# Kernel optimization log

Measured on AMD Instinct MI355X. Metric: run time of the kernel, lower is better.

## Reference

```python
import math
import jax, jax.numpy as jnp
from jax import lax
import numpy as np

B, DIM, H, W = 8, 256, 64, 64
D_STATE, D_CONV, EXPAND = 16, 4, 2
D_INNER = EXPAND * DIM
DT_RANK = math.ceil(DIM / 16)
POS_LEN = 16
EPS = 1e-5
GN_GROUPS = 32


def setup_inputs() -> dict:
    key = jax.random.key(0)
    ks = iter(jax.random.split(key, 24))
    rn = lambda shape, s=0.02: jax.random.normal(next(ks), shape, jnp.float32) * s
    inp = {}
    inp["x"] = jax.random.normal(next(ks), (B, DIM, H, W), jnp.float32)
    inp["pos_emb"] = rn((1, DIM, POS_LEN), 1.0)
    inp["ln_g"] = jnp.ones((DIM,), jnp.float32)
    inp["ln_b"] = jnp.zeros((DIM,), jnp.float32)
    inp["m_in_w"] = rn((2, 2 * D_INNER, DIM))
    inp["m_conv_w"] = rn((2, D_INNER, D_CONV), 0.1)
    inp["m_conv_b"] = jnp.zeros((2, D_INNER), jnp.float32)
    inp["m_xproj_w"] = rn((2, DT_RANK + 2 * D_STATE, D_INNER))
    inp["m_dt_w"] = rn((2, D_INNER, DT_RANK), 0.1)
    inp["m_dt_b"] = rn((2, D_INNER), 0.1)
    inp["m_A_log"] = jnp.tile(jnp.log(jnp.arange(1, D_STATE + 1, dtype=jnp.float32))[None, None, :], (2, D_INNER, 1))
    inp["m_D"] = jnp.ones((2, D_INNER), jnp.float32)
    inp["m_out_w"] = rn((2, DIM, D_INNER))
    inp["proj_w"] = rn((DIM, 2 * DIM))
    inp["proj_b"] = jnp.zeros((DIM,), jnp.float32)
    inp["up_dw_w"] = rn((DIM, 1, 3, 3), 0.1)
    inp["up_bn1_g"] = jnp.ones((DIM,), jnp.float32)
    inp["up_bn1_b"] = jnp.zeros((DIM,), jnp.float32)
    inp["up_pw_w"] = rn((DIM, DIM), 0.05)
    inp["up_bn2_g"] = jnp.ones((DIM,), jnp.float32)
    inp["up_bn2_b"] = jnp.zeros((DIM,), jnp.float32)
    inp["down_pw_w"] = rn((DIM, DIM), 0.05)
    inp["down_bn_g"] = jnp.ones((DIM,), jnp.float32)
    inp["down_bn_b"] = jnp.zeros((DIM,), jnp.float32)
    inp["gn_g"] = jnp.ones((DIM,), jnp.float32)
    inp["gn_b"] = jnp.zeros((DIM,), jnp.float32)
    return inp


def reference(x, pos_emb, ln_g, ln_b, m_in_w, m_conv_w, m_conv_b, m_xproj_w, m_dt_w, m_dt_b,
              m_A_log, m_D, m_out_w, proj_w, proj_b, up_dw_w, up_bn1_g, up_bn1_b, up_pw_w,
              up_bn2_g, up_bn2_b, down_pw_w, down_bn_g, down_bn_b, gn_g, gn_b):
    Bx, C, Hh, Ww = x.shape

    def ln(t):  # LayerNorm over last dim (shared self.norm)
        m = jnp.mean(t, -1, keepdims=True)
        v = jnp.mean((t - m) ** 2, -1, keepdims=True)
        return (t - m) * lax.rsqrt(v + EPS) * ln_g + ln_b

    def bn(t, g, b):  # BatchNorm2d in eval mode with default running stats (mean 0, var 1)
        return t * (g / jnp.sqrt(1.0 + EPS))[None, :, None, None] + b[None, :, None, None]

    def gn(t):  # GroupNorm(32, C), shared params (self.bn)
        Bn, Cn, Hn, Wn = t.shape
        tg = t.reshape(Bn, GN_GROUPS, Cn // GN_GROUPS, Hn, Wn)
        m = jnp.mean(tg, (2, 3, 4), keepdims=True)
        v = jnp.mean((tg - m) ** 2, (2, 3, 4), keepdims=True)
        tg = (tg - m) * lax.rsqrt(v + EPS)
        return tg.reshape(Bn, Cn, Hn, Wn) * gn_g[None, :, None, None] + gn_b[None, :, None, None]

    def interp_pos(N):  # F.interpolate(pos_embed, size=N, mode='linear', align_corners=False)
        coords = jnp.maximum((jnp.arange(N, dtype=jnp.float32) + 0.5) * (POS_LEN / N) - 0.5, 0.0)
        i0 = jnp.floor(coords).astype(jnp.int32)
        i1 = jnp.minimum(i0 + 1, POS_LEN - 1)
        wgt = coords - i0.astype(jnp.float32)
        return pos_emb[:, :, i0] * (1.0 - wgt) + pos_emb[:, :, i1] * wgt  # (1,C,N)

    def pe_branch(vals, idx, N):  # vals (B,C,N); indices interp at same size = identity
        t = vals + interp_pos(N) + idx.astype(jnp.float32)
        return ln(jnp.swapaxes(t, 1, 2))  # (B,N,C)

    def mamba(u, d):  # standard mamba_ssm selective scan; u (B,L,C)
        xz = jnp.einsum('blc,ic->bli', u, m_in_w[d])
        xh, zg = jnp.split(xz, 2, -1)
        xc = lax.conv_general_dilated(jnp.swapaxes(xh, 1, 2), m_conv_w[d][:, None, :], (1,),
                                      [(D_CONV - 1, 0)], feature_group_count=D_INNER,
                                      dimension_numbers=('NCH', 'OIH', 'NCH'))
        xc = jnp.swapaxes(jax.nn.silu(xc + m_conv_b[d][None, :, None]), 1, 2)  # (B,L,di)
        dbl = jnp.einsum('bld,ed->ble', xc, m_xproj_w[d])
        dt = dbl[..., :DT_RANK]
        Bm = dbl[..., DT_RANK:DT_RANK + D_STATE]
        Cm = dbl[..., DT_RANK + D_STATE:]
        dt = jax.nn.softplus(jnp.einsum('blr,dr->bld', dt, m_dt_w[d]) + m_dt_b[d])  # (B,L,di)
        A = -jnp.exp(m_A_log[d])  # (di,ds)
        dA = jnp.exp(dt[..., None] * A)  # (B,L,di,ds)
        dBx = dt[..., None] * Bm[:, :, None, :] * xc[..., None]

        def step(h, inps):
            dA_t, dBx_t, C_t = inps
            h = dA_t * h + dBx_t
            return h, jnp.einsum('bds,bs->bd', h, C_t)

        h0 = jnp.zeros((u.shape[0], D_INNER, D_STATE), u.dtype)
        _, ys = lax.scan(step, h0, (jnp.swapaxes(dA, 0, 1), jnp.swapaxes(dBx, 0, 1), jnp.swapaxes(Cm, 0, 1)))
        y = jnp.swapaxes(ys, 0, 1) + xc * m_D[d]
        y = y * jax.nn.silu(zg)
        return jnp.einsum('bld,od->blo', y, m_out_w[d])

    # z branch: depthwise ConvTranspose2d(k3,s2,p1,op1) + BN + ReLU + pw conv + BN, then ReLU6
    z = lax.conv_general_dilated(x, jnp.flip(up_dw_w, (2, 3)), (1, 1), [(1, 2), (1, 2)],
                                 lhs_dilation=(2, 2), feature_group_count=C,
                                 dimension_numbers=('NCHW', 'OIHW', 'NCHW'))  # (B,C,2H,2W)
    z = jax.nn.relu(bn(z, up_bn1_g, up_bn1_b))
    z = jnp.einsum('bchw,oc->bohw', z, up_pw_w)
    z = jnp.clip(bn(z, up_bn2_g, up_bn2_b), 0.0, 6.0)

    col_max = pe_branch(jnp.max(x, 2), jnp.argmax(x, 2), Ww)
    col_min = pe_branch(jnp.min(x, 2), jnp.argmin(x, 2), Ww)
    row_max = pe_branch(jnp.max(x, 3), jnp.argmax(x, 3), Hh)
    row_min = pe_branch(jnp.min(x, 3), jnp.argmin(x, 3), Hh)
    result_max = jnp.concatenate([col_max, row_max], 1)  # (B, W+H, C)
    result_min = jnp.concatenate([col_min, row_min], 1)

    fm_max = ln(mamba(result_max, 0))
    fm_min = ln(mamba(result_min, 0))
    bm_max = ln(mamba(jnp.flip(result_max, 1), 1))
    bm_min = ln(mamba(jnp.flip(result_min, 1), 1))

    res_max = jnp.concatenate([fm_max, jnp.flip(bm_max, 1)], -1) @ proj_w.T + proj_b
    res_min = jnp.concatenate([fm_min, jnp.flip(bm_min, 1)], -1) @ proj_w.T + proj_b
    res_max = ln(res_max)[:, :, None, :]  # (B,L,1,C)
    res_min = ln(res_min)[:, None, :, :]  # (B,1,L,C)

    res = jnp.transpose(res_max + res_min, (0, 3, 1, 2))  # (B,C,L,L), L=H+W=2H
    res = jnp.clip(res + 3.0, 0.0, 6.0) / 6.0 * z  # h_sigmoid gate
    res = gn(res)
    res = jnp.einsum('bchw,oc->bohw', res[:, :, ::2, ::2], down_pw_w)  # pw conv stride 2
    res = bn(res, down_bn_g, down_bn_b)
    res = gn(res)
    res = res + x
    res = gn(res)
    return res
```

## Files before the change

kernel.cpp:

```cpp
#include <hip/hip_runtime.h>
#include <hip/hip_bf16.h>
#include <math.h>

typedef __hip_bfloat16 bf16;
typedef __attribute__((ext_vector_type(8))) short short8_t;
typedef __attribute__((ext_vector_type(4))) short short4_t;
typedef __attribute__((ext_vector_type(4))) float f32x4_t;

#define EPSV 1e-5f
#define BNSC 0.99999500003749968f

__device__ __forceinline__ float bf2f(bf16 v){ return __bfloat162float(v); }
__device__ __forceinline__ bf16 f2bf(float v){ return __float2bfloat16(v); }

__device__ __forceinline__ float blk_sum(float v, float* sm){
  int tid = threadIdx.x;
  #pragma unroll
  for(int o=32;o>0;o>>=1) v += __shfl_down(v, o, 64);
  if((tid&63)==0) sm[tid>>6] = v;
  __syncthreads();
  float s = 0.f;
  int nw = blockDim.x>>6;
  for(int i=0;i<nw;i++) s += sm[i];
  __syncthreads();
  return s;
}

__device__ __forceinline__ float softplusf(float x){
  return (x > 20.f) ? x : __logf(1.f + __expf(x));
}
__device__ __forceinline__ float siluf(float x){
  return x / (1.f + __expf(-x));
}

__global__ void prep_weights(const float* __restrict__ in_w, const float* __restrict__ out_w,
                             const float* __restrict__ pw_w, const float* __restrict__ dpw_w,
                             const float* __restrict__ proj_w,
                             bf16* __restrict__ Winb, bf16* __restrict__ Woutb,
                             bf16* __restrict__ Wub, bf16* __restrict__ Wdb,
                             float* __restrict__ PT, float* __restrict__ gacc){
  int idx = blockIdx.x*256 + threadIdx.x;
  if(idx < 1536) gacc[idx] = 0.f;
  if(idx < 524288){ Winb[idx] = f2bf(in_w[idx]); return; }
  if(idx < 786432){ int i=idx-524288; Woutb[i] = f2bf(out_w[i]); return; }
  if(idx < 851968){ int i=idx-786432; Wub[i] = f2bf(pw_w[i]); return; }
  if(idx < 917504){ int i=idx-851968; Wdb[i] = f2bf(dpw_w[i]); return; }
  int k = idx - 917504;
  int i = k >> 9, j = k & 511;
  PT[j*256 + i] = proj_w[k];
}

__global__ __launch_bounds__(256)
void r1_reduce_pe(const float* __restrict__ x, const float* __restrict__ pe,
                  float* __restrict__ pmax, float* __restrict__ pmin){
  __shared__ float tile[64*65];
  int bc = blockIdx.x;
  int b = bc >> 8, c = bc & 255;
  const float* xp = x + ((size_t)bc << 12);
  for(int i=threadIdx.x; i<4096; i+=256)
    tile[(i>>6)*65 + (i&63)] = xp[i];
  __syncthreads();
  int wv = threadIdx.x >> 6, t = threadIdx.x & 63;
  if(wv >= 2) return;
  float coords = fmaxf((t + 0.5f)*0.25f - 0.5f, 0.f);
  int i0 = (int)floorf(coords);
  int i1 = min(i0+1, 15);
  float wg = coords - (float)i0;
  float pos = pe[c*16+i0]*(1.f-wg) + pe[c*16+i1]*wg;
  if(wv == 0){
    float cmx=-3.4e38f, cmn=3.4e38f; int cax=0, can=0;
    for(int h=0;h<64;h++){
      float v = tile[h*65 + t];
      if(v > cmx){ cmx=v; cax=h; }
      if(v < cmn){ cmn=v; can=h; }
    }
    size_t base_col = ((size_t)b*128 + t)*256 + c;
    pmax[base_col] = cmx + pos + (float)cax;
    pmin[base_col] = cmn + pos + (float)can;
  } else {
    float rmx=-3.4e38f, rmn=3.4e38f; int rax=0, ran=0;
    for(int w=0;w<64;w++){
      float v = tile[t*65 + w];
      if(v > rmx){ rmx=v; rax=w; }
      if(v < rmn){ rmn=v; ran=w; }
    }
    size_t base_row = ((size_t)b*128 + 64 + t)*256 + c;
    pmax[base_row] = rmx + pos + (float)rax;
    pmin[base_row] = rmn + pos + (float)ran;
  }
}

__global__ void ln_rows2(float* __restrict__ bufA, float* __restrict__ bufB,
                         const float* __restrict__ g, const float* __restrict__ bb,
                         bf16* __restrict__ boutA, bf16* __restrict__ boutB){
  __shared__ float sm[8];
  int row = blockIdx.x, t = threadIdx.x;
  float* buf; bf16* bout;
  if(row < 1024){ buf = bufA; bout = boutA; }
  else { buf = bufB; bout = boutB; row -= 1024; }
  float v = buf[(size_t)row*256 + t];
  float m = blk_sum(v, sm) * (1.f/256.f);
  float dv = v - m;
  float var = blk_sum(dv*dv, sm) * (1.f/256.f);
  float r = dv * rsqrtf(var + EPSV) * g[t] + bb[t];
  buf[(size_t)row*256 + t] = r;
  if(bout) bout[(size_t)row*256 + t] = f2bf(r);
}

__global__ __launch_bounds__(256,2)
void m1_mfma(const bf16* __restrict__ ubmax, const bf16* __restrict__ ubmin,
             const bf16* __restrict__ Win, float* __restrict__ xz){
  __shared__ bf16 att[64*264];
  int bx = blockIdx.x;
  int it = bx & 3, lt = (bx>>2)&1, b = (bx>>3)&7, r = bx>>6;
  int d = r & 1;
  const bf16* u = (r < 2) ? ubmax : ubmin;
  int flip = r & 1;
  int t = threadIdx.x;
  {
    int pr = t>>5, cc = (t&31)*8;
    #pragma unroll
    for(int i=0;i<8;i++){
      int p = pr + i*8;
      int l = lt*64 + p;
      int le = flip ? (127 - l) : l;
      short8_t v = *(const short8_t*)((const short*)u + ((size_t)(b*128 + le))*256 + cc);
      *(short8_t*)&att[p*264 + cc] = v;
    }
  }
  __syncthreads();
  int wv = t>>6, lane = t&63, quad = lane>>4, l16 = lane&15;
  int m0 = wv*64;
  f32x4_t acc[4][4];
  #pragma unroll
  for(int ms=0;ms<4;ms++)
    #pragma unroll
    for(int ns=0;ns<4;ns++) acc[ms][ns] = (f32x4_t){0.f,0.f,0.f,0.f};
  const short* wbase = (const short*)Win + ((size_t)d*1024 + it*256)*256;
  for(int k0=0;k0<256;k0+=32){
    short8_t afr[4], bfr[4];
    #pragma unroll
    for(int ms=0;ms<4;ms++)
      afr[ms] = *(const short8_t*)(wbase + (size_t)(m0 + ms*16 + l16)*256 + k0 + quad*8);
    #pragma unroll
    for(int ns=0;ns<4;ns++)
      bfr[ns] = *(const short8_t*)&att[(ns*16 + l16)*264 + k0 + quad*8];
    #pragma unroll
    for(int ms=0;ms<4;ms++)
      #pragma unroll
      for(int ns=0;ns<4;ns++)
        acc[ms][ns] = __builtin_amdgcn_mfma_f32_16x16x32_bf16(afr[ms], bfr[ns], acc[ms][ns], 0,0,0);
  }
  int rb = r*8 + b;
  #pragma unroll
  for(int ns=0;ns<4;ns++){
    int l = lt*64 + ns*16 + l16;
    float* dst = xz + ((size_t)rb*128 + l)*1024 + it*256;
    #pragma unroll
    for(int ms=0;ms<4;ms++){
      int i = m0 + ms*16 + quad*4;
      *(f32x4_t*)(dst + i) = acc[ms][ns];
    }
  }
}

#define LSEG 8
__global__ __launch_bounds__(256)
void m234(const float* __restrict__ xz, const float* __restrict__ cw,
          const float* __restrict__ cb, const float* __restrict__ xproj,
          const float* __restrict__ dtw, const float* __restrict__ dtbias,
          float* __restrict__ xc, float* __restrict__ dbl, float* __restrict__ dt){
  __shared__ float xzs[(LSEG+3)*512];
  __shared__ float xcs[LSEG*512];
  __shared__ float pbuf[LSEG*96];
  __shared__ float dblrow[LSEG*48];
  int bx = blockIdx.x;
  int rb = bx >> 4, seg = bx & 15;
  int l0 = seg * LSEG;
  int d = (rb >> 3) & 1;
  int t = threadIdx.x;
  #pragma unroll
  for(int j=0; j<(LSEG+3)*512/256; j++){
    int i = t + j*256;
    int r = i >> 9, dd = i & 511;
    int ls = l0 - 3 + r;
    xzs[i] = (ls >= 0) ? xz[((size_t)rb*128 + ls)*1024 + dd] : 0.f;
  }
  __syncthreads();
  #pragma unroll
  for(int j=0; j<(LSEG*512)/256; j++){
    int i = t + j*256;
    int lr = i >> 9, dd = i & 511;
    f32x4_t wv = *(const f32x4_t*)(cw + (size_t)(d*512 + dd)*4);
    float s = cb[d*512 + dd];
    s += xzs[(lr+0)*512 + dd]*wv[0];
    s += xzs[(lr+1)*512 + dd]*wv[1];
    s += xzs[(lr+2)*512 + dd]*wv[2];
    s += xzs[(lr+3)*512 + dd]*wv[3];
    s = siluf(s);
    xcs[i] = s;
    xc[((size_t)(rb*128 + l0 + lr))*512 + dd] = s;
  }
  __syncthreads();
  #pragma unroll
  for(int j=0; j<3; j++){
    int id = t + j*256;
    int row = id / 96;
    int rem = id - row*96;
    int e = rem >> 1, part = rem & 1;
    const float* wp = xproj + ((size_t)(d*48 + e)*512) + part*256;
    const float* xr = xcs + row*512 + part*256;
    float s = 0.f;
    #pragma unroll 4
    for(int k4=0; k4<64; k4++){
      f32x4_t wv = *(const f32x4_t*)(wp + k4*4);
      f32x4_t xv = *(const f32x4_t*)(xr + k4*4);
      s += wv[0]*xv[0] + wv[1]*xv[1] + wv[2]*xv[2] + wv[3]*xv[3];
    }
    pbuf[id] = s;
  }
  __syncthreads();
  for(int i=t; i<LSEG*48; i+=256){
    float s = pbuf[2*i] + pbuf[2*i+1];
    dblrow[i] = s;
    int row = i / 48, e = i - row*48;
    dbl[((size_t)(rb*128 + l0 + row))*48 + e] = s;
  }
  __syncthreads();
  #pragma unroll
  for(int j=0; j<(LSEG*512)/256; j++){
    int i = t + j*256;
    int row = i >> 9, dd = i & 511;
    const float* wp = dtw + (size_t)(d*512 + dd)*16;
    const float* dr = dblrow + row*48;
    float s = dtbias[d*512 + dd];
    #pragma unroll
    for(int r4=0; r4<4; r4++){
      f32x4_t wv = *(const f32x4_t*)(wp + r4*4);
      s += dr[r4*4+0]*wv[0] + dr[r4*4+1]*wv[1] + dr[r4*4+2]*wv[2] + dr[r4*4+3]*wv[3];
    }
    dt[((size_t)(rb*128 + l0 + row))*512 + dd] = softplusf(s);
  }
}

__global__ void m5_passA(const float* __restrict__ dt, const float* __restrict__ xc,
                         const float* __restrict__ dbl, const float* __restrict__ Alog,
                         float* __restrict__ P, float* __restrict__ Hl){
  int bx = blockIdx.x;
  int seg = bx & 7, half = (bx>>3)&1, rb = bx>>4;
  int dd = half*256 + threadIdx.x;
  int d = (rb>>3)&1;
  float A[16], h[16], pr[16];
  #pragma unroll
  for(int s=0;s<16;s++){
    A[s] = -__expf(Alog[(size_t)(d*512 + dd)*16 + s]);
    h[s] = 0.f; pr[s] = 1.f;
  }
  int l0 = seg*16;
  for(int l=l0;l<l0+16;l++){
    size_t row = (size_t)rb*128 + l;
    float dtv = dt[row*512 + dd];
    float xcv = xc[row*512 + dd];
    float bx_ = dtv*xcv;
    const float* dr = dbl + row*48;
    #pragma unroll
    for(int s=0;s<16;s++){
      float dA = __expf(dtv*A[s]);
      pr[s] *= dA;
      h[s] = dA*h[s] + bx_*dr[16+s];
    }
  }
  size_t o = ((size_t)(rb*8 + seg)*512 + dd)*16;
  #pragma unroll
  for(int s=0;s<16;s+=4){
    *(f32x4_t*)(P  + o + s) = (f32x4_t){pr[s],pr[s+1],pr[s+2],pr[s+3]};
    *(f32x4_t*)(Hl + o + s) = (f32x4_t){h[s],h[s+1],h[s+2],h[s+3]};
  }
}

__global__ void m5_passB(const float* __restrict__ dt, const float* __restrict__ xc,
                         const float* __restrict__ dbl, const float* __restrict__ xz,
                         const float* __restrict__ Alog, const float* __restrict__ Dp,
                         const float* __restrict__ P, const float* __restrict__ Hl,
                         bf16* __restrict__ ybb){
  int bx = blockIdx.x;
  int seg = bx & 7, half = (bx>>3)&1, rb = bx>>4;
  int dd = half*256 + threadIdx.x;
  int d = (rb>>3)&1;
  float A[16], h[16];
  #pragma unroll
  for(int s=0;s<16;s++){
    A[s] = -__expf(Alog[(size_t)(d*512 + dd)*16 + s]);
    h[s] = 0.f;
  }
  for(int j=0;j<seg;j++){
    size_t o = ((size_t)(rb*8 + j)*512 + dd)*16;
    #pragma unroll
    for(int s=0;s<16;s+=4){
      f32x4_t pv = *(const f32x4_t*)(P + o + s);
      f32x4_t hv = *(const f32x4_t*)(Hl + o + s);
      h[s]   = pv[0]*h[s]   + hv[0];
      h[s+1] = pv[1]*h[s+1] + hv[1];
      h[s+2] = pv[2]*h[s+2] + hv[2];
      h[s+3] = pv[3]*h[s+3] + hv[3];
    }
  }
  float Dv = Dp[d*512 + dd];
  int l0 = seg*16;
  for(int l=l0;l<l0+16;l++){
    size_t row = (size_t)rb*128 + l;
    float dtv = dt[row*512 + dd];
    float xcv = xc[row*512 + dd];
    float zgv = xz[row*1024 + 512 + dd];
    const float* dr = dbl + row*48;
    float bx_ = dtv*xcv;
    float y = 0.f;
    #pragma unroll
    for(int s=0;s<16;s++){
      h[s] = __expf(dtv*A[s])*h[s] + bx_*dr[16+s];
      y += h[s]*dr[32+s];
    }
    ybb[row*512 + dd] = f2bf((y + xcv*Dv) * siluf(zgv));
  }
}

__global__ __launch_bounds__(256,2)
void m6_mfma(const bf16* __restrict__ ybb, const bf16* __restrict__ Wout,
             const float* __restrict__ lng, const float* __restrict__ lnb,
             float* __restrict__ mo){
  __shared__ char smem[64*264*4];
  bf16* ybt = (bf16*)smem;
  float* fbuf = (float*)smem;
  int bx = blockIdx.x;
  int lt = bx & 1, b = (bx>>1)&7, r = bx>>4;
  int d = r & 1, rb = r*8 + b;
  size_t rowbase = (size_t)rb*128 + lt*64;
  int t = threadIdx.x;
  for(int i=t;i<4096;i+=256){
    int row = i>>6, c8 = (i&63)*8;
    short8_t v = *(const short8_t*)((const short*)ybb + (rowbase + row)*512 + c8);
    *(short8_t*)&ybt[row*520 + c8] = v;
  }
  __syncthreads();
  int wv = t>>6, lane = t&63, quad = lane>>4, l16 = lane&15;
  int m0 = wv*64;
  f32x4_t acc[4][4];
  #pragma unroll
  for(int ms=0;ms<4;ms++)
    #pragma unroll
    for(int ns=0;ns<4;ns++) acc[ms][ns] = (f32x4_t){0.f,0.f,0.f,0.f};
  const short* wbase = (const short*)Wout + (size_t)d*256*512;
  for(int k0=0;k0<512;k0+=32){
    short8_t afr[4], bfr[4];
    #pragma unroll
    for(int ms=0;ms<4;ms++)
      afr[ms] = *(const short8_t*)(wbase + (size_t)(m0 + ms*16 + l16)*512 + k0 + quad*8);
    #pragma unroll
    for(int ns=0;ns<4;ns++)
      bfr[ns] = *(const short8_t*)&ybt[(ns*16 + l16)*520 + k0 + quad*8];
    #pragma unroll
    for(int ms=0;ms<4;ms++)
      #pragma unroll
      for(int ns=0;ns<4;ns++)
        acc[ms][ns] = __builtin_amdgcn_mfma_f32_16x16x32_bf16(afr[ms], bfr[ns], acc[ms][ns], 0,0,0);
  }
  __syncthreads();
  #pragma unroll
  for(int ns=0;ns<4;ns++){
    int row = ns*16 + l16;
    #pragma unroll
    for(int ms=0;ms<4;ms++){
      int o = m0 + ms*16 + quad*4;
      *(f32x4_t*)(fbuf + row*264 + o) = acc[ms][ns];
    }
  }
  __syncthreads();
  {
    int row = t >> 2, part = t & 3;
    const float* fr = fbuf + row*264;
    float s = 0.f;
    #pragma unroll 8
    for(int j=0;j<64;j++){
      int col = part*64 + ((j + part*16) & 63);
      s += fr[col];
    }
    s += __shfl_xor(s, 1, 64);
    s += __shfl_xor(s, 2, 64);
    float m = s * (1.f/256.f);
    float q = 0.f;
    #pragma unroll 8
    for(int j=0;j<64;j++){
      int col = part*64 + ((j + part*16) & 63);
      float dv = fr[col] - m;
      q += dv*dv;
    }
    q += __shfl_xor(q, 1, 64);
    q += __shfl_xor(q, 2, 64);
    float rs = rsqrtf(q*(1.f/256.f) + EPSV);
    float* dst = mo + (rowbase + row)*256;
    for(int j=0;j<64;j++){
      int col = part*64 + j;
      dst[col] = (fr[col] - m)*rs*lng[col] + lnb[col];
    }
  }
}

__global__ void m7_proj(const float* __restrict__ mo, const float* __restrict__ PT,
                        const float* __restrict__ pb, const float* __restrict__ lng,
                        const float* __restrict__ lnb, float* __restrict__ resm,
                        float* __restrict__ resn){
  __shared__ float ct[16*512];
  __shared__ float fbuf[16*264];
  int bx = blockIdx.x;
  int tt = bx >> 6, rem = bx & 63, b = rem >> 3, lt = rem & 7;
  int fr_ = tt*2, br = tt*2 + 1;
  for(int i=threadIdx.x;i<16*512;i+=256){
    int lr = i >> 9, k = i & 511;
    int l = lt*16 + lr;
    ct[i] = (k < 256)
      ? mo[(((size_t)(fr_*8+b)*128) + l)*256 + k]
      : mo[(((size_t)(br*8+b)*128) + (127-l))*256 + (k-256)];
  }
  __syncthreads();
  float acc[16];
  #pragma unroll
  for(int q=0;q<16;q++) acc[q] = 0.f;
  int t = threadIdx.x;
  for(int k=0;k<512;k++){
    float pv = PT[(size_t)k*256 + t];
    #pragma unroll
    for(int q=0;q<16;q++) acc[q] += pv * ct[(q<<9) + k];
  }
  float bias = pb[t];
  #pragma unroll
  for(int q=0;q<16;q++) fbuf[q*264 + t] = acc[q] + bias;
  __syncthreads();
  float* dstbuf = tt ? resn : resm;
  if(t < 64){
    int row = t >> 2, part = t & 3;
    const float* fr = fbuf + row*264;
    float s = 0.f;
    for(int j=0;j<64;j++){
      int col = part*64 + ((j + part*16) & 63);
      s += fr[col];
    }
    s += __shfl_xor(s, 1, 64);
    s += __shfl_xor(s, 2, 64);
    float m = s * (1.f/256.f);
    float q = 0.f;
    for(int j=0;j<64;j++){
      int col = part*64 + ((j + part*16) & 63);
      float dv = fr[col] - m;
      q += dv*dv;
    }
    q += __shfl_xor(q, 1, 64);
    q += __shfl_xor(q, 2, 64);
    float rs = rsqrtf(q*(1.f/256.f) + EPSV);
    float* dst = dstbuf + ((size_t)b*128 + lt*16 + row)*256;
    for(int j=0;j<64;j++){
      int col = part*64 + j;
      dst[col] = (fr[col] - m)*rs*lng[col] + lnb[col];
    }
  }
}

__global__ __launch_bounds__(256)
void k1_deconv_T(const float* __restrict__ x, const float* __restrict__ wdw,
                 const float* __restrict__ g1, const float* __restrict__ b1,
                 bf16* __restrict__ zT){
  __shared__ float in[2*64*33];
  __shared__ bf16 ot[64*80];
  int bx = blockIdx.x;
  int cb = bx & 3, half = (bx>>2)&1, h = (bx>>3)&127, b = bx>>10;
  int c0 = cb*64, w0 = half*64, iw0 = w0>>1;
  int h_odd = h & 1;
  int ihA = h_odd ? (h-1)>>1 : h>>1;
  int ihB = (h+1)>>1;
  bool hasB = h_odd && (ihB < 64);
  for(int i = threadIdx.x; i < 4224; i += 256){
    int row = i / 2112;
    int rem = i - row*2112;
    int c = rem / 33;
    int iw = rem - c*33;
    int ihl = row ? ihB : ihA;
    bool valid = (iw0 + iw < 64) && (row == 0 || hasB);
    in[i] = valid ? x[(((size_t)b*256 + c0 + c)<<12) + (ihl<<6) + iw0 + iw] : 0.f;
  }
  __syncthreads();
  int c = threadIdx.x & 63, g = threadIdx.x >> 6;
  const float* wp = wdw + (c0+c)*9;
  int khA3 = h_odd ? 6 : 3;
  float wA0 = wp[khA3], wA1 = wp[khA3+1], wA2 = wp[khA3+2];
  float wB0 = wp[0],    wB1 = wp[1],      wB2 = wp[2];
  float scale = g1[c0+c]*BNSC, bias = b1[c0+c];
  const float* inA = in + c*33;
  const float* inB = in + 2112 + c*33;
  #pragma unroll
  for(int i=0;i<16;i++){
    int wi = g*16 + i;
    float s;
    if(!(i&1)){
      int iw = wi>>1;
      s = inA[iw]*wA1 + inB[iw]*wB1;
    } else {
      int iwa = (wi-1)>>1, iwb = (wi+1)>>1;
      s = inA[iwa]*wA2 + inA[iwb]*wA0 + inB[iwa]*wB2 + inB[iwb]*wB0;
    }
    ot[wi*80 + c] = f2bf(fmaxf(s*scale + bias, 0.f));
  }
  __syncthreads();
  int rr = threadIdx.x >> 3;
  int co = (threadIdx.x & 7) * 8;
  size_t obase = (((size_t)b*16384) + (size_t)h*128 + w0)*256 + c0;
  #pragma unroll
  for(int pass=0; pass<2; pass++){
    int wi = rr + pass*32;
    short8_t v = *(const short8_t*)&ot[wi*80 + co];
    *(short8_t*)((short*)zT + obase + (size_t)wi*256 + co) = v;
  }
}

__global__ __launch_bounds__(256,4)
void k2_mfma(const bf16* __restrict__ zT, const bf16* __restrict__ Wub,
             const float* __restrict__ g2, const float* __restrict__ b2,
             const float* __restrict__ resm, const float* __restrict__ resn,
             bf16* __restrict__ resT, float* __restrict__ gsum1, float* __restrict__ gssq1){
  __shared__ bf16 zt[64*264];
  __shared__ float gn_s[32], gn_q[32];
  int b = blockIdx.y;
  int p0 = blockIdx.x*64;
  int t = threadIdx.x;
  if(t < 32){ gn_s[t] = 0.f; gn_q[t] = 0.f; }
  {
    const short* src = (const short*)zT + (((size_t)b*16384 + p0)*256);
    int pr = t>>5;
    int cc = (t&31)*8;
    #pragma unroll
    for(int i=0;i<8;i++){
      int p = pr + i*8;
      short8_t v = *(const short8_t*)(src + (size_t)p*256 + cc);
      *(short8_t*)&zt[p*264 + cc] = v;
    }
  }
  __syncthreads();
  int wv = t>>6, lane = t&63, quad = lane>>4, l16 = lane&15;
  int m0 = wv*64;
  f32x4_t acc[4][4];
  #pragma unroll
  for(int ms=0;ms<4;ms++)
    #pragma unroll
    for(int ns=0;ns<4;ns++) acc[ms][ns] = (f32x4_t){0.f,0.f,0.f,0.f};
  const short* wp = (const short*)Wub + (size_t)(m0 + l16)*256 + quad*8;
  short8_t afr[4];
  #pragma unroll
  for(int ms=0;ms<4;ms++) afr[ms] = *(const short8_t*)(wp + (size_t)ms*16*256);
  for(int k0=0;k0<256;k0+=32){
    short8_t anext[4];
    if(k0 + 32 < 256){
      #pragma unroll
      for(int ms=0;ms<4;ms++)
        anext[ms] = *(const short8_t*)(wp + (size_t)ms*16*256 + k0 + 32);
    }
    short8_t bfr[4];
    #pragma unroll
    for(int ns=0;ns<4;ns++)
      bfr[ns] = *(const short8_t*)&zt[(ns*16 + l16)*264 + k0 + quad*8];
    #pragma unroll
    for(int ms=0;ms<4;ms++)
      #pragma unroll
      for(int ns=0;ns<4;ns++)
        acc[ms][ns] = __builtin_amdgcn_mfma_f32_16x16x32_bf16(afr[ms], bfr[ns], acc[ms][ns], 0,0,0);
    #pragma unroll
    for(int ms=0;ms<4;ms++) afr[ms] = anext[ms];
  }
  __syncthreads();
  float sg[4], qg[4];
  #pragma unroll
  for(int ms=0;ms<4;ms++){ sg[ms]=0.f; qg[ms]=0.f; }
  #pragma unroll
  for(int ns=0;ns<4;ns++){
    int pl = ns*16 + l16;
    int p = p0 + pl;
    int hh = p>>7, ww = p&127;
    const float* rm = resm + ((size_t)b*128+hh)*256;
    const float* rn = resn + ((size_t)b*128+ww)*256;
    #pragma unroll
    for(int ms=0;ms<4;ms++){
      int o = m0 + ms*16 + quad*4;
      f32x4_t a = acc[ms][ns];
      f32x4_t gv = *(const f32x4_t*)(g2+o);
      f32x4_t bv = *(const f32x4_t*)(b2+o);
      f32x4_t rmv = *(const f32x4_t*)(rm+o);
      f32x4_t rnv = *(const f32x4_t*)(rn+o);
      alignas(8) bf16 ov[4];
      #pragma unroll
      for(int r=0;r<4;r++){
        float zv = a[r]*(gv[r]*BNSC) + bv[r];
        zv = fminf(fmaxf(zv, 0.f), 6.f);
        float gate = fminf(fmaxf(rmv[r]+rnv[r]+3.f, 0.f), 6.f)*(1.f/6.f);
        float vo = zv*gate;
        ov[r] = f2bf(vo);
        sg[ms] += vo;
        qg[ms] += vo*vo;
      }
      *(short4_t*)&zt[pl*264 + o] = *(const short4_t*)ov;
    }
  }
  #pragma unroll
  for(int ms=0;ms<4;ms++){
    float S = sg[ms], Q = qg[ms];
    S += __shfl_xor(S, 1, 64);  Q += __shfl_xor(Q, 1, 64);
    S += __shfl_xor(S, 2, 64);  Q += __shfl_xor(Q, 2, 64);
    S += __shfl_xor(S, 4, 64);  Q += __shfl_xor(Q, 4, 64);
    S += __shfl_xor(S, 8, 64);  Q += __shfl_xor(Q, 8, 64);
    if(l16 == 0){
      int o = m0 + ms*16 + quad*4;
      atomicAdd(&gn_s[o>>3], S);
      atomicAdd(&gn_q[o>>3], Q);
    }
  }
  __syncthreads();
  if(t < 32){
    atomicAdd(&gsum1[b*32 + t], gn_s[t]);
    atomicAdd(&gssq1[b*32 + t], gn_q[t]);
  }
  {
    short* dst = (short*)resT + ((size_t)b*16384 + p0)*256;
    #pragma unroll
    for(int it=0; it<8; it++){
      int slot = t + it*256;
      int row = slot >> 5;
      int co = (slot & 31)*8;
      short8_t v = *(const short8_t*)&zt[row*264 + co];
      *(short8_t*)(dst + (size_t)row*256 + co) = v;
    }
  }
}

__global__ __launch_bounds__(256,2)
void k4_mfma(const bf16* __restrict__ resT, const bf16* __restrict__ Wdb,
             const float* __restrict__ gsum1, const float* __restrict__ gssq1,
             const float* __restrict__ gng, const float* __restrict__ gnb,
             const float* __restrict__ dbg, const float* __restrict__ dbb,
             float* __restrict__ t1, float* __restrict__ gsum2, float* __restrict__ gssq2){
  __shared__ bf16 at[128*264];
  __shared__ float sc[256], sb[256];
  __shared__ float stm[32], str[32];
  int b = blockIdx.y;
  int q0 = blockIdx.x*128;
  int t = threadIdx.x;
  if(t < 32){
    float m = gsum1[b*32+t] * (1.f/131072.f);
    float var = gssq1[b*32+t] * (1.f/131072.f) - m*m;
    stm[t] = m;
    str[t] = rsqrtf(var + EPSV);
  }
  __syncthreads();
  {
    int cch = t, g = cch>>3;
    float m = stm[g], rs = str[g];
    float s = rs*gng[cch];
    sc[cch] = s; sb[cch] = gnb[cch] - m*s;
  }
  __syncthreads();
  {
    int pr = t>>5;
    int cc = (t&31)*8;
    #pragma unroll
    for(int i=0;i<16;i++){
      int q = pr + i*8;
      int qq = q0 + q;
      int y = qq>>6, xw = qq&63;
      size_t srow = ((size_t)b*16384 + (size_t)y*256 + xw*2)*256;
      short8_t v = *(const short8_t*)((const short*)resT + srow + cc);
      const bf16* vv = (const bf16*)&v;
      alignas(16) bf16 ov[8];
      #pragma unroll
      for(int j=0;j<8;j++) ov[j] = f2bf(bf2f(vv[j])*sc[cc+j] + sb[cc+j]);
      *(short8_t*)&at[q*264 + cc] = *(const short8_t*)ov;
    }
  }
  __syncthreads();
  int wv = t>>6, lane = t&63, quad = lane>>4, l16 = lane&15;
  int n0 = wv*64;
  f32x4_t acc[8][4];
  #pragma unroll
  for(int ms=0;ms<8;ms++)
    #pragma unroll
    for(int ns=0;ns<4;ns++) acc[ms][ns] = (f32x4_t){0.f,0.f,0.f,0.f};
  const short* wp = (const short*)Wdb + (size_t)(n0 + l16)*256 + quad*8;
  short8_t bfr[4];
  #pragma unroll
  for(int ns=0;ns<4;ns++) bfr[ns] = *(const short8_t*)(wp + (size_t)ns*16*256);
  for(int k0=0;k0<256;k0+=32){
    short8_t bnext[4];
    if(k0 + 32 < 256){
      #pragma unroll
      for(int ns=0;ns<4;ns++)
        bnext[ns] = *(const short8_t*)(wp + (size_t)ns*16*256 + k0 + 32);
    }
    short8_t afr[8];
    #pragma unroll
    for(int ms=0;ms<8;ms++)
      afr[ms] = *(const short8_t*)&at[(ms*16 + l16)*264 + k0 + quad*8];
    #pragma unroll
    for(int ms=0;ms<8;ms++)
      #pragma unroll
      for(int ns=0;ns<4;ns++)
        acc[ms][ns] = __builtin_amdgcn_mfma_f32_16x16x32_bf16(afr[ms], bfr[ns], acc[ms][ns], 0,0,0);
    #pragma unroll
    for(int ns=0;ns<4;ns++) bfr[ns] = bnext[ns];
  }
  #pragma unroll
  for(int ns=0;ns<4;ns++){
    int o = n0 + ns*16 + l16;
    float s2 = dbg[o]*BNSC, bb2 = dbb[o];
    float* dst = t1 + (((size_t)b*256 + o) << 12);
    float s_=0.f, q_=0.f;
    #pragma unroll
    for(int ms=0;ms<8;ms++){
      int ps = q0 + ms*16 + quad*4;
      f32x4_t a = acc[ms][ns];
      f32x4_t ov;
      #pragma unroll
      for(int r=0;r<4;r++){
        ov[r] = a[r]*s2 + bb2;
        s_ += ov[r];
        q_ += ov[r]*ov[r];
      }
      *(f32x4_t*)(dst + ps) = ov;
    }
    #pragma unroll
    for(int msk=1; msk<=4; msk<<=1){
      s_ += __shfl_xor(s_, msk, 64);
      q_ += __shfl_xor(q_, msk, 64);
    }
    s_ += __shfl_xor(s_, 16, 64);
    q_ += __shfl_xor(q_, 16, 64);
    s_ += __shfl_xor(s_, 32, 64);
    q_ += __shfl_xor(q_, 32, 64);
    if(((l16 & 7) == 0) && (quad == 0)){
      atomicAdd(&gsum2[b*32 + (o>>3)], s_);
      atomicAdd(&gssq2[b*32 + (o>>3)], q_);
    }
  }
}

__global__ void k6_gn_add(float* __restrict__ t1, const float* __restrict__ x,
                          const float* __restrict__ gsum2, const float* __restrict__ gssq2,
                          const float* __restrict__ gng, const float* __restrict__ gnb,
                          float* __restrict__ gsum3, float* __restrict__ gssq3){
  __shared__ float sm[8];
  int i4 = blockIdx.x*256 + threadIdx.x;
  int idx = i4 << 2;
  int c = (idx >> 12) & 255, b = idx >> 20, g = c >> 3;
  float m2 = gsum2[b*32+g] * (1.f/32768.f);
  float var = gssq2[b*32+g] * (1.f/32768.f) - m2*m2;
  float rs = rsqrtf(var + EPSV);
  float scl = rs*gng[c], off = gnb[c] - m2*scl;
  f32x4_t tv = *(const f32x4_t*)(t1 + idx);
  f32x4_t xv = *(const f32x4_t*)(x + idx);
  f32x4_t ov;
  float S = 0.f, Q = 0.f;
  #pragma unroll
  for(int r=0;r<4;r++){
    float v = tv[r]*scl + off + xv[r];
    ov[r] = v;
    S += v; Q += v*v;
  }
  *(f32x4_t*)(t1 + idx) = ov;
  S = blk_sum(S, sm);
  Q = blk_sum(Q, sm);
  if(threadIdx.x == 0){
    atomicAdd(&gsum3[b*32 + g], S);
    atomicAdd(&gssq3[b*32 + g], Q);
  }
}

__global__ void k8_gn_out(const float* __restrict__ t1, const float* __restrict__ gsum3,
                          const float* __restrict__ gssq3, const float* __restrict__ gng,
                          const float* __restrict__ gnb, float* __restrict__ out){
  int i4 = blockIdx.x*256 + threadIdx.x;
  int idx = i4 << 2;
  int c = (idx >> 12) & 255, b = idx >> 20, g = c >> 3;
  float m = gsum3[b*32+g] * (1.f/32768.f);
  float var = gssq3[b*32+g] * (1.f/32768.f) - m*m;
  float rs = rsqrtf(var + EPSV);
  float scl = rs*gng[c], off = gnb[c] - m*scl;
  f32x4_t tv = *(const f32x4_t*)(t1 + idx);
  f32x4_t ov;
  #pragma unroll
  for(int r=0;r<4;r++) ov[r] = tv[r]*scl + off;
  *(f32x4_t*)(out + idx) = ov;
}

extern "C" void kernel_launch(void* const* d_in, const int* in_sizes, int n_in,
                              void* d_out, int out_size, void* d_ws, size_t ws_size,
                              hipStream_t stream){
  const float* x      = (const float*)d_in[0];
  const float* pos    = (const float*)d_in[1];
  const float* ln_g   = (const float*)d_in[2];
  const float* ln_b   = (const float*)d_in[3];
  const float* in_w   = (const float*)d_in[4];
  const float* conv_w = (const float*)d_in[5];
  const float* conv_b = (const float*)d_in[6];
  const float* xproj  = (const float*)d_in[7];
  const float* dt_w   = (const float*)d_in[8];
  const float* dt_b   = (const float*)d_in[9];
  const float* A_log  = (const float*)d_in[10];
  const float* Dp     = (const float*)d_in[11];
  const float* out_w  = (const float*)d_in[12];
  const float* proj_w = (const float*)d_in[13];
  const float* proj_b = (const float*)d_in[14];
  const float* dw_w   = (const float*)d_in[15];
  const float* bn1g   = (const float*)d_in[16];
  const float* bn1b   = (const float*)d_in[17];
  const float* pw_w   = (const float*)d_in[18];
  const float* bn2g   = (const float*)d_in[19];
  const float* bn2b   = (const float*)d_in[20];
  const float* dpw_w  = (const float*)d_in[21];
  const float* dbng   = (const float*)d_in[22];
  const float* dbnb   = (const float*)d_in[23];
  const float* gng    = (const float*)d_in[24];
  const float* gnb    = (const float*)d_in[25];
  float* out = (float*)d_out;

  float* ws = (float*)d_ws;
  bf16*  resT = (bf16*)ws;
  bf16*  zT   = (bf16*)(ws + 16777216);
  float* scanP = ws + 16777216;
  float* scanH = ws + 16777216 + 2097152;
  float* zone = ws + 33554432;
  float* xz   = zone;
  float* xc   = xz  + 4194304;
  float* dbl  = xc  + 2097152;
  float* dtb  = dbl + 196608;
  bf16*  ybb  = (bf16*)(dtb + 2097152);
  float* t1   = zone;
  float* mo   = zone + 9633792;
  float* resm = mo   + 1048576;
  float* resn = resm + 262144;
  float* pmax = resn + 262144;
  float* pmin = pmax + 262144;
  float* PT   = pmin + 262144;
  bf16*  ubmax= (bf16*)(PT + 131072);
  bf16*  ubmin= (bf16*)(PT + 131072 + 131072);
  bf16*  Winb = (bf16*)(PT + 131072 + 262144);
  bf16*  Woutb= (bf16*)(PT + 131072 + 524288);
  bf16*  Wub  = (bf16*)(PT + 131072 + 655360);
  bf16*  Wdb  = (bf16*)(PT + 131072 + 688128);
  float* gacc = PT + 131072 + 720896;
  float* gsum1 = gacc,        *gssq1 = gacc + 256;
  float* gsum2 = gacc + 512,  *gssq2 = gacc + 768;
  float* gsum3 = gacc + 1024, *gssq3 = gacc + 1280;

  prep_weights<<<4096,256,0,stream>>>(in_w, out_w, pw_w, dpw_w, proj_w,
                                      Winb, Woutb, Wub, Wdb, PT, gacc);

  r1_reduce_pe<<<2048,256,0,stream>>>(x, pos, pmax, pmin);
  ln_rows2<<<2048,256,0,stream>>>(pmax, pmin, ln_g, ln_b, ubmax, ubmin);

  m1_mfma<<<256,256,0,stream>>>(ubmax, ubmin, Winb, xz);
  m234<<<512,256,0,stream>>>(xz, conv_w, conv_b, xproj, dt_w, dt_b, xc, dbl, dtb);
  m5_passA<<<512,256,0,stream>>>(dtb, xc, dbl, A_log, scanP, scanH);
  m5_passB<<<512,256,0,stream>>>(dtb, xc, dbl, xz, A_log, Dp, scanP, scanH, ybb);
  m6_mfma<<<64,256,0,stream>>>(ybb, Woutb, ln_g, ln_b, mo);
  m7_proj<<<128,256,0,stream>>>(mo, PT, proj_b, ln_g, ln_b, resm, resn);

  k1_deconv_T<<<8192,256,0,stream>>>(x, dw_w, bn1g, bn1b, zT);
  k2_mfma<<<dim3(256,8),256,0,stream>>>(zT, Wub, bn2g, bn2b, resm, resn, resT,
                                        gsum1, gssq1);

  k4_mfma<<<dim3(32,8),256,0,stream>>>(resT, Wdb, gsum1, gssq1,
                                       gng, gnb, dbng, dbnb, t1, gsum2, gssq2);

  k6_gn_add<<<8192,256,0,stream>>>(t1, x, gsum2, gssq2, gng, gnb, gsum3, gssq3);
  k8_gn_out<<<8192,256,0,stream>>>(t1, gsum3, gssq3, gng, gnb, out);
}
```

Before: 517.3 us.

## Write only stride-2 subsampled gated output from k2 and enlarge tile to a row

k2 now processes a full 128-pixel row per block (64x128 accumulator tile per wave), caches the row's resm vector in shared memory, and writes only the even-row, even-column pixels that the stride-2 downsample consumes into a compact buffer. k4 reads that compact buffer contiguously instead of gathering strided rows. GroupNorm statistics are still accumulated over all pixels. This removes three quarters of the intermediate bf16 write traffic, but doubles shared memory and register use in k2, which lowers occupancy.

```diff
diff --git a/kernel.cpp b/kernel.cpp
--- a/kernel.cpp
+++ b/kernel.cpp
@@ -520,23 +520,29 @@
   }
 }
 
-__global__ __launch_bounds__(256,4)
+__global__ __launch_bounds__(256,2)
 void k2_mfma(const bf16* __restrict__ zT, const bf16* __restrict__ Wub,
              const float* __restrict__ g2, const float* __restrict__ b2,
              const float* __restrict__ resm, const float* __restrict__ resn,
-             bf16* __restrict__ resT, float* __restrict__ gsum1, float* __restrict__ gssq1){
-  __shared__ bf16 zt[64*264];
+             bf16* __restrict__ resS, float* __restrict__ gsum1, float* __restrict__ gssq1){
+  __shared__ bf16 zt[128*264];
+  __shared__ float rm_s[256];
   __shared__ float gn_s[32], gn_q[32];
   int b = blockIdx.y;
-  int p0 = blockIdx.x*64;
+  int p0 = blockIdx.x*128;
+  int h = p0 >> 7;
   int t = threadIdx.x;
   if(t < 32){ gn_s[t] = 0.f; gn_q[t] = 0.f; }
+  if(t >= 64 && t < 128){
+    int tt = t - 64;
+    *(f32x4_t*)&rm_s[tt*4] = *(const f32x4_t*)(resm + ((size_t)b*128 + h)*256 + tt*4);
+  }
   {
     const short* src = (const short*)zT + (((size_t)b*16384 + p0)*256);
     int pr = t>>5;
     int cc = (t&31)*8;
     #pragma unroll
-    for(int i=0;i<8;i++){
+    for(int i=0;i<16;i++){
       int p = pr + i*8;
       short8_t v = *(const short8_t*)(src + (size_t)p*256 + cc);
       *(short8_t*)&zt[p*264 + cc] = v;
@@ -545,11 +551,11 @@
   __syncthreads();
   int wv = t>>6, lane = t&63, quad = lane>>4, l16 = lane&15;
   int m0 = wv*64;
-  f32x4_t acc[4][4];
+  f32x4_t acc[4][8];
   #pragma unroll
   for(int ms=0;ms<4;ms++)
     #pragma unroll
-    for(int ns=0;ns<4;ns++) acc[ms][ns] = (f32x4_t){0.f,0.f,0.f,0.f};
+    for(int ns=0;ns<8;ns++) acc[ms][ns] = (f32x4_t){0.f,0.f,0.f,0.f};
   const short* wp = (const short*)Wub + (size_t)(m0 + l16)*256 + quad*8;
   short8_t afr[4];
   #pragma unroll
@@ -561,36 +567,35 @@
       for(int ms=0;ms<4;ms++)
         anext[ms] = *(const short8_t*)(wp + (size_t)ms*16*256 + k0 + 32);
     }
-    short8_t bfr[4];
-    #pragma unroll
-    for(int ns=0;ns<4;ns++)
+    short8_t bfr[8];
+    #pragma unroll
+    for(int ns=0;ns<8;ns++)
       bfr[ns] = *(const short8_t*)&zt[(ns*16 + l16)*264 + k0 + quad*8];
     #pragma unroll
     for(int ms=0;ms<4;ms++)
       #pragma unroll
-      for(int ns=0;ns<4;ns++)
+      for(int ns=0;ns<8;ns++)
         acc[ms][ns] = __builtin_amdgcn_mfma_f32_16x16x32_bf16(afr[ms], bfr[ns], acc[ms][ns], 0,0,0);
     #pragma unroll
     for(int ms=0;ms<4;ms++) afr[ms] = anext[ms];
   }
   __syncthreads();
+  bool h_even = ((h & 1) == 0);
   float sg[4], qg[4];
   #pragma unroll
   for(int ms=0;ms<4;ms++){ sg[ms]=0.f; qg[ms]=0.f; }
   #pragma unroll
-  for(int ns=0;ns<4;ns++){
+  for(int ns=0;ns<8;ns++){
     int pl = ns*16 + l16;
-    int p = p0 + pl;
-    int hh = p>>7, ww = p&127;
-    const float* rm = resm + ((size_t)b*128+hh)*256;
-    const float* rn = resn + ((size_t)b*128+ww)*256;
+    const float* rn = resn + ((size_t)b*128 + pl)*256;
+    bool store = h_even && ((pl & 1) == 0);
     #pragma unroll
     for(int ms=0;ms<4;ms++){
       int o = m0 + ms*16 + quad*4;
       f32x4_t a = acc[ms][ns];
       f32x4_t gv = *(const f32x4_t*)(g2+o);
       f32x4_t bv = *(const f32x4_t*)(b2+o);
-      f32x4_t rmv = *(const f32x4_t*)(rm+o);
+      f32x4_t rmv = *(const f32x4_t*)&rm_s[o];
       f32x4_t rnv = *(const f32x4_t*)(rn+o);
       alignas(8) bf16 ov[4];
       #pragma unroll
@@ -603,7 +608,7 @@
         sg[ms] += vo;
         qg[ms] += vo*vo;
       }
-      *(short4_t*)&zt[pl*264 + o] = *(const short4_t*)ov;
+      if(store) *(short4_t*)&zt[pl*264 + o] = *(const short4_t*)ov;
     }
   }
   #pragma unroll
@@ -624,21 +629,21 @@
     atomicAdd(&gsum1[b*32 + t], gn_s[t]);
     atomicAdd(&gssq1[b*32 + t], gn_q[t]);
   }
-  {
-    short* dst = (short*)resT + ((size_t)b*16384 + p0)*256;
+  if(h_even){
+    short* dst = (short*)resS + ((size_t)b*4096 + (h>>1)*64)*256;
     #pragma unroll
     for(int it=0; it<8; it++){
       int slot = t + it*256;
       int row = slot >> 5;
       int co = (slot & 31)*8;
-      short8_t v = *(const short8_t*)&zt[row*264 + co];
+      short8_t v = *(const short8_t*)&zt[(row*2)*264 + co];
       *(short8_t*)(dst + (size_t)row*256 + co) = v;
     }
   }
 }
 
 __global__ __launch_bounds__(256,2)
-void k4_mfma(const bf16* __restrict__ resT, const bf16* __restrict__ Wdb,
+void k4_mfma(const bf16* __restrict__ resS, const bf16* __restrict__ Wdb,
              const float* __restrict__ gsum1, const float* __restrict__ gssq1,
              const float* __restrict__ gng, const float* __restrict__ gnb,
              const float* __restrict__ dbg, const float* __restrict__ dbb,
@@ -666,13 +671,11 @@
   {
     int pr = t>>5;
     int cc = (t&31)*8;
+    const short* src = (const short*)resS + ((size_t)b*4096 + q0)*256;
     #pragma unroll
     for(int i=0;i<16;i++){
       int q = pr + i*8;
-      int qq = q0 + q;
-      int y = qq>>6, xw = qq&63;
-      size_t srow = ((size_t)b*16384 + (size_t)y*256 + xw*2)*256;
-      short8_t v = *(const short8_t*)((const short*)resT + srow + cc);
+      short8_t v = *(const short8_t*)(src + (size_t)q*256 + cc);
       const bf16* vv = (const bf16*)&v;
       alignas(16) bf16 ov[8];
       #pragma unroll
@@ -826,7 +829,7 @@
   float* out = (float*)d_out;
 
   float* ws = (float*)d_ws;
-  bf16*  resT = (bf16*)ws;
+  bf16*  resS = (bf16*)ws;
   bf16*  zT   = (bf16*)(ws + 16777216);
   float* scanP = ws + 16777216;
   float* scanH = ws + 16777216 + 2097152;
@@ -868,10 +871,10 @@
   m7_proj<<<128,256,0,stream>>>(mo, PT, proj_b, ln_g, ln_b, resm, resn);
 
   k1_deconv_T<<<8192,256,0,stream>>>(x, dw_w, bn1g, bn1b, zT);
-  k2_mfma<<<dim3(256,8),256,0,stream>>>(zT, Wub, bn2g, bn2b, resm, resn, resT,
+  k2_mfma<<<dim3(128,8),256,0,stream>>>(zT, Wub, bn2g, bn2b, resm, resn, resS,
                                         gsum1, gssq1);
 
-  k4_mfma<<<dim3(32,8),256,0,stream>>>(resT, Wdb, gsum1, gssq1,
+  k4_mfma<<<dim3(32,8),256,0,stream>>>(resS, Wdb, gsum1, gssq1,
                                        gng, gnb, dbng, dbnb, t1, gsum2, gssq2);
 
   k6_gn_add<<<8192,256,0,stream>>>(t1, x, gsum2, gssq2, gng, gnb, gsum3, gssq3);
```

Measured after the change: 502.4 us. -2.9%, faster.
